# Optimization experiments

Measured on AMD Instinct MI355X. Metric: run time of the kernel, lower is better.

The kernel has to match this reference:

```python
import jax, jax.numpy as jnp
import numpy as np

NEG_INF = -1e10  # matches torch masked_fill_ value -10000000000.0


def setup_inputs() -> dict:
    key = jax.random.key(0)
    kq, kk, kv, kd, km = jax.random.split(key, 5)
    B, H, S, D = 4, 8, 2048, 64
    Q = jax.random.normal(kq, (B, H, S, D), dtype=jnp.float32)
    K = jax.random.normal(kk, (B, H, S, D), dtype=jnp.float32)
    V = jax.random.normal(kv, (B, H, S, D), dtype=jnp.float32)
    dist_factor = jax.random.uniform(kd, (B, H, S, S), dtype=jnp.float32)
    attn_mask = jax.random.randint(km, (B, H, S, S), 0, 2).astype(jnp.bool_)
    return {"Q": Q, "K": K, "V": V, "dist_factor": dist_factor, "attn_mask": attn_mask}


def reference(Q, K, V, dist_factor, attn_mask):
    d_k = K.shape[-1]
    # [B,H,S,S] raw scores, scaled by 1/sqrt(d_k) then by distance factor
    scores = jnp.einsum("bhqd,bhkd->bhqk", Q, K) / np.sqrt(d_k).astype(jnp.float32)
    scores = dist_factor * scores
    scores = jnp.where(attn_mask, jnp.asarray(NEG_INF, scores.dtype), scores)
    attn = jax.nn.softmax(scores, axis=-1)
    context = jnp.einsum("bhqk,bhkd->bhqd", attn, V)
    return (context, attn)
```

## Files before the change

kernel.cpp:

```cpp
#include <hip/hip_runtime.h>


typedef float v4f __attribute__((ext_vector_type(4)));
typedef _Float16 v8h __attribute__((ext_vector_type(8)));

#define SEQ 2048
#define DH  64
#define TQ  8
#define TK  64
#define NKT (SEQ / TK)
#define NBH 32
#define PLANE ((size_t)NBH * NKT * 256)

__device__ inline v8h cvt8(float4 a, float4 b) {
    v8h h;
    h[0] = (_Float16)a.x; h[1] = (_Float16)a.y; h[2] = (_Float16)a.z; h[3] = (_Float16)a.w;
    h[4] = (_Float16)b.x; h[5] = (_Float16)b.y; h[6] = (_Float16)b.z; h[7] = (_Float16)b.w;
    return h;
}

__global__ __launch_bounds__(256)
void prep_kernel(const float* __restrict__ Kg, const float* __restrict__ Vg,
                 v8h* __restrict__ W)
{
    const int kt   = blockIdx.x;
    const int bh   = blockIdx.y;
    const int tid  = (int)threadIdx.x;
    const int wave = tid >> 6;
    const int lane = tid & 63;
    const int quad = lane >> 4;
    const int l16  = lane & 15;
    const int k0   = kt * TK;

    const size_t bh_off = (size_t)bh * SEQ * DH;
    const size_t fi     = ((size_t)bh * NKT + kt) * 256 + tid;

    const float* kr = Kg + bh_off + (size_t)(k0 + wave * 16 + l16) * DH + quad * 8;
    W[fi]         = cvt8(((const float4*)kr)[0], ((const float4*)kr)[1]);
    W[PLANE + fi] = cvt8(((const float4*)(kr + 32))[0], ((const float4*)(kr + 32))[1]);

    const float* vc = Vg + bh_off + (size_t)(k0 + quad * 8) * DH + wave * 16 + l16;
    v8h v0, v1;
#pragma unroll
    for (int j = 0; j < 8; ++j) {
        v0[j] = (_Float16)vc[(size_t)j * DH];
        v1[j] = (_Float16)vc[(size_t)(j + 32) * DH];
    }
    W[2 * PLANE + fi] = v0;
    W[3 * PLANE + fi] = v1;
}

template<bool USE_WS>
__global__ __launch_bounds__(256, 4)
void dsda_kernel(const float* __restrict__ Qg, const float* __restrict__ Kg,
                 const float* __restrict__ Vg, const float* __restrict__ distg,
                 const int* __restrict__ maskg, const v8h* __restrict__ W,
                 float* __restrict__ ctx_out, float* __restrict__ attn_out)
{
    const int qt   = blockIdx.x;
    const int bh   = blockIdx.y;
    const int q0   = qt * TQ;
    const int tid  = (int)threadIdx.x;
    const int wave = tid >> 6;
    const int lane = tid & 63;
    const int quad = lane >> 4;
    const int l16  = lane & 15;

    __shared__ __align__(16) _Float16 e_smem[TQ * SEQ];
    __shared__ float rs[TQ];
    if (tid < TQ) rs[tid] = 0.f;

    const size_t bh_off  = (size_t)bh * SEQ;
    const float* Qb = Qg + bh_off * DH;
    const float* Kb = Kg + bh_off * DH;
    const float* Vb = Vg + bh_off * DH;
    const size_t dm_base = (bh_off + (size_t)q0) * SEQ;

    v8h aq0 = {}, aq1 = {};
    if (l16 < TQ) {
        const float* qrow = Qb + (size_t)(q0 + l16) * DH;
        const float4* p0 = (const float4*)(qrow + quad * 8);
        const float4* p1 = (const float4*)(qrow + 32 + quad * 8);
        aq0 = cvt8(p0[0], p0[1]);
        aq1 = cvt8(p1[0], p1[1]);
    }

    v4f acc_pv = {0.f, 0.f, 0.f, 0.f};
    float rsum[4] = {0.f, 0.f, 0.f, 0.f};
    const size_t fbase = (size_t)bh * NKT * 256 + tid;

#define LOAD_FRAGS(KT, B0, B1, B2, B3) do {                                   \
        const size_t fi_ = fbase + (size_t)(KT) * 256;                        \
        B0 = W[fi_]; B1 = W[PLANE + fi_];                                     \
        B2 = W[2 * PLANE + fi_]; B3 = W[3 * PLANE + fi_];                     \
    } while (0)

#define LOAD_DM(KT, DV, MV) do {                                              \
        if (quad < 2) {                                                       \
            const int kc_ = (KT) * TK + wave * 16 + l16;                      \
            _Pragma("unroll")                                                 \
            for (int r_ = 0; r_ < 4; ++r_) {                                  \
                const size_t idx_ = dm_base + (size_t)(quad * 4 + r_) * SEQ + kc_; \
                DV[r_] = __builtin_nontemporal_load(&distg[idx_]);            \
                MV[r_] = __builtin_nontemporal_load(&maskg[idx_]);            \
            }                                                                 \
        }                                                                     \
    } while (0)

    if constexpr (USE_WS) {
        v8h bk0_c, bk1_c, bv0_c, bv1_c;
        float dv_c[4] = {}; int mv_c[4] = {};
        LOAD_FRAGS(0, bk0_c, bk1_c, bv0_c, bv1_c);
        LOAD_DM(0, dv_c, mv_c);

#pragma unroll 2
        for (int kt = 0; kt < NKT; ++kt) {
            const int k0 = kt * TK;

            const int ktn = (kt + 1 < NKT) ? kt + 1 : 0;
            v8h bk0_n, bk1_n, bv0_n, bv1_n;
            float dv_n[4] = {}; int mv_n[4] = {};
            LOAD_FRAGS(ktn, bk0_n, bk1_n, bv0_n, bv1_n);
            LOAD_DM(ktn, dv_n, mv_n);

            v4f accs = {0.f, 0.f, 0.f, 0.f};
            accs = __builtin_amdgcn_mfma_f32_16x16x32_f16(aq0, bk0_c, accs, 0, 0, 0);
            accs = __builtin_amdgcn_mfma_f32_16x16x32_f16(aq1, bk1_c, accs, 0, 0, 0);

            if (quad < 2) {
                const int kc = k0 + wave * 16 + l16;
#pragma unroll
                for (int r = 0; r < 4; ++r) {
                    const int row = quad * 4 + r;
                    const float sc = accs[r] * 0.125f * dv_c[r];
                    const float e  = mv_c[r] ? 0.f : __expf(sc);
                    rsum[r] += e;
                    *(_Float16*)((char*)e_smem + (row * (SEQ * 2) + ((kc * 2) ^ (row << 4)))) = (_Float16)e;
                }
            }

            asm volatile("s_waitcnt lgkmcnt(0)" ::: "memory");
            __builtin_amdgcn_s_barrier();
            asm volatile("" ::: "memory");

            v8h ap0 = {}, ap1 = {};
            if (l16 < TQ) {
                const int b0 = l16 * (SEQ * 2) + (((k0 + quad * 8) * 2) ^ (l16 << 4));
                const int b1 = l16 * (SEQ * 2) + (((k0 + 32 + quad * 8) * 2) ^ (l16 << 4));
                ap0 = *(const v8h*)((const char*)e_smem + b0);
                ap1 = *(const v8h*)((const char*)e_smem + b1);
            }
            acc_pv = __builtin_amdgcn_mfma_f32_16x16x32_f16(ap0, bv0_c, acc_pv, 0, 0, 0);
            acc_pv = __builtin_amdgcn_mfma_f32_16x16x32_f16(ap1, bv1_c, acc_pv, 0, 0, 0);

            bk0_c = bk0_n; bk1_c = bk1_n; bv0_c = bv0_n; bv1_c = bv1_n;
#pragma unroll
            for (int r = 0; r < 4; ++r) { dv_c[r] = dv_n[r]; mv_c[r] = mv_n[r]; }
        }
    } else {
        for (int kt = 0; kt < NKT; ++kt) {
            const int k0 = kt * TK;
            v8h bk0, bk1, bv0, bv1;
            const float* kr = Kb + (size_t)(k0 + wave * 16 + l16) * DH + quad * 8;
            bk0 = cvt8(((const float4*)kr)[0], ((const float4*)kr)[1]);
            bk1 = cvt8(((const float4*)(kr + 32))[0], ((const float4*)(kr + 32))[1]);
            const float* vc = Vb + (size_t)(k0 + quad * 8) * DH + wave * 16 + l16;
#pragma unroll
            for (int j = 0; j < 8; ++j) {
                bv0[j] = (_Float16)vc[(size_t)j * DH];
                bv1[j] = (_Float16)vc[(size_t)(j + 32) * DH];
            }
            float dv[4] = {}; int mv[4] = {};
            LOAD_DM(kt, dv, mv);

            v4f accs = {0.f, 0.f, 0.f, 0.f};
            accs = __builtin_amdgcn_mfma_f32_16x16x32_f16(aq0, bk0, accs, 0, 0, 0);
            accs = __builtin_amdgcn_mfma_f32_16x16x32_f16(aq1, bk1, accs, 0, 0, 0);

            if (quad < 2) {
                const int kc = k0 + wave * 16 + l16;
#pragma unroll
                for (int r = 0; r < 4; ++r) {
                    const int row = quad * 4 + r;
                    const float sc = accs[r] * 0.125f * dv[r];
                    const float e  = mv[r] ? 0.f : __expf(sc);
                    rsum[r] += e;
                    *(_Float16*)((char*)e_smem + (row * (SEQ * 2) + ((kc * 2) ^ (row << 4)))) = (_Float16)e;
                }
            }
            __syncthreads();

            v8h ap0 = {}, ap1 = {};
            if (l16 < TQ) {
                const int b0 = l16 * (SEQ * 2) + (((k0 + quad * 8) * 2) ^ (l16 << 4));
                const int b1 = l16 * (SEQ * 2) + (((k0 + 32 + quad * 8) * 2) ^ (l16 << 4));
                ap0 = *(const v8h*)((const char*)e_smem + b0);
                ap1 = *(const v8h*)((const char*)e_smem + b1);
            }
            acc_pv = __builtin_amdgcn_mfma_f32_16x16x32_f16(ap0, bv0, acc_pv, 0, 0, 0);
            acc_pv = __builtin_amdgcn_mfma_f32_16x16x32_f16(ap1, bv1, acc_pv, 0, 0, 0);
        }
    }

    if (quad < 2) {
#pragma unroll
        for (int r = 0; r < 4; ++r) {
            float v = rsum[r];
            v += __shfl_xor(v, 1);
            v += __shfl_xor(v, 2);
            v += __shfl_xor(v, 4);
            v += __shfl_xor(v, 8);
            if (l16 == 0) atomicAdd(&rs[quad * 4 + r], v);
        }
    }
    __syncthreads();

    if (quad < 2) {
#pragma unroll
        for (int r = 0; r < 4; ++r) {
            const int row = quad * 4 + r;
            const float inv = 1.f / rs[row];
            ctx_out[(bh_off + (size_t)(q0 + row)) * DH + wave * 16 + l16] = acc_pv[r] * inv;
        }
    }

    {
        const int r  = tid >> 5;
        const int tt = tid & 31;
        const float invr = 1.f / rs[r];
        float* arow = attn_out + dm_base + (size_t)r * SEQ;
#pragma unroll
        for (int c = 0; c < 8; ++c) {
            const int col = c * 256 + tt * 8;
            const int b   = r * (SEQ * 2) + ((col * 2) ^ (r << 4));
            v8h e8 = *(const v8h*)((const char*)e_smem + b);
            v4f f0, f1;
            f0[0] = (float)e8[0] * invr; f0[1] = (float)e8[1] * invr;
            f0[2] = (float)e8[2] * invr; f0[3] = (float)e8[3] * invr;
            f1[0] = (float)e8[4] * invr; f1[1] = (float)e8[5] * invr;
            f1[2] = (float)e8[6] * invr; f1[3] = (float)e8[7] * invr;
            __builtin_nontemporal_store(f0, (v4f*)(arow + col));
            __builtin_nontemporal_store(f1, (v4f*)(arow + col) + 1);
        }
    }
}

extern "C" void kernel_launch(void* const* d_in, const int* in_sizes, int n_in,
                              void* d_out, int out_size, void* d_ws, size_t ws_size,
                              hipStream_t stream) {
    const float* Q    = (const float*)d_in[0];
    const float* K    = (const float*)d_in[1];
    const float* V    = (const float*)d_in[2];
    const float* dist = (const float*)d_in[3];
    const int*   mask = (const int*)d_in[4];

    float* ctx  = (float*)d_out;
    float* attn = (float*)d_out + (size_t)4 * 8 * 2048 * 64;

    const size_t need = 4 * PLANE * sizeof(v8h);
    if (d_ws != nullptr && ws_size >= need) {
        hipLaunchKernelGGL(prep_kernel, dim3(NKT, NBH), dim3(256), 0, stream,
                           K, V, (v8h*)d_ws);
        hipLaunchKernelGGL((dsda_kernel<true>), dim3(SEQ / TQ, NBH), dim3(256), 0, stream,
                           Q, K, V, dist, mask, (const v8h*)d_ws, ctx, attn);
    } else {
        hipLaunchKernelGGL((dsda_kernel<false>), dim3(SEQ / TQ, NBH), dim3(256), 0, stream,
                           Q, K, V, dist, mask, (const v8h*)nullptr, ctx, attn);
    }
}
```

Baseline: 1.401 ms.

## Use 16-row query tiles to fill all MFMA rows

Raises the query tile from 8 to 16 rows so the 16x16 MFMA tiles are fully used rather than half-masked. Each K/V fragment load and prep-buffer read now serves twice as many queries, and the grid is halved. Shared memory per block doubles to 64KB, and launch bounds drop to 2 blocks per CU. That reduces occupancy, which may hurt the latency hiding needed for the streaming dist/mask reads.

```diff
diff --git a/kernel.cpp b/kernel.cpp
--- a/kernel.cpp
+++ b/kernel.cpp
@@ -6,7 +6,7 @@
 
 #define SEQ 2048
 #define DH  64
-#define TQ  8
+#define TQ  16
 #define TK  64
 #define NKT (SEQ / TK)
 #define NBH 32
@@ -51,7 +51,7 @@
 }
 
 template<bool USE_WS>
-__global__ __launch_bounds__(256, 4)
+__global__ __launch_bounds__(256, 2)
 void dsda_kernel(const float* __restrict__ Qg, const float* __restrict__ Kg,
                  const float* __restrict__ Vg, const float* __restrict__ distg,
                  const int* __restrict__ maskg, const v8h* __restrict__ W,
@@ -76,8 +76,8 @@
     const float* Vb = Vg + bh_off * DH;
     const size_t dm_base = (bh_off + (size_t)q0) * SEQ;
 
-    v8h aq0 = {}, aq1 = {};
-    if (l16 < TQ) {
+    v8h aq0, aq1;
+    {
         const float* qrow = Qb + (size_t)(q0 + l16) * DH;
         const float4* p0 = (const float4*)(qrow + quad * 8);
         const float4* p1 = (const float4*)(qrow + 32 + quad * 8);
@@ -96,20 +96,18 @@
     } while (0)
 
 #define LOAD_DM(KT, DV, MV) do {                                              \
-        if (quad < 2) {                                                       \
-            const int kc_ = (KT) * TK + wave * 16 + l16;                      \
-            _Pragma("unroll")                                                 \
-            for (int r_ = 0; r_ < 4; ++r_) {                                  \
-                const size_t idx_ = dm_base + (size_t)(quad * 4 + r_) * SEQ + kc_; \
-                DV[r_] = __builtin_nontemporal_load(&distg[idx_]);            \
-                MV[r_] = __builtin_nontemporal_load(&maskg[idx_]);            \
-            }                                                                 \
+        const int kc_ = (KT) * TK + wave * 16 + l16;                          \
+        _Pragma("unroll")                                                     \
+        for (int r_ = 0; r_ < 4; ++r_) {                                      \
+            const size_t idx_ = dm_base + (size_t)(quad * 4 + r_) * SEQ + kc_; \
+            DV[r_] = __builtin_nontemporal_load(&distg[idx_]);                \
+            MV[r_] = __builtin_nontemporal_load(&maskg[idx_]);                \
         }                                                                     \
     } while (0)
 
     if constexpr (USE_WS) {
         v8h bk0_c, bk1_c, bv0_c, bv1_c;
-        float dv_c[4] = {}; int mv_c[4] = {};
+        float dv_c[4]; int mv_c[4];
         LOAD_FRAGS(0, bk0_c, bk1_c, bv0_c, bv1_c);
         LOAD_DM(0, dv_c, mv_c);
 
@@ -119,7 +117,7 @@
 
             const int ktn = (kt + 1 < NKT) ? kt + 1 : 0;
             v8h bk0_n, bk1_n, bv0_n, bv1_n;
-            float dv_n[4] = {}; int mv_n[4] = {};
+            float dv_n[4]; int mv_n[4];
             LOAD_FRAGS(ktn, bk0_n, bk1_n, bv0_n, bv1_n);
             LOAD_DM(ktn, dv_n, mv_n);
 
@@ -127,7 +125,7 @@
             accs = __builtin_amdgcn_mfma_f32_16x16x32_f16(aq0, bk0_c, accs, 0, 0, 0);
             accs = __builtin_amdgcn_mfma_f32_16x16x32_f16(aq1, bk1_c, accs, 0, 0, 0);
 
-            if (quad < 2) {
+            {
                 const int kc = k0 + wave * 16 + l16;
 #pragma unroll
                 for (int r = 0; r < 4; ++r) {
@@ -135,7 +133,7 @@
                     const float sc = accs[r] * 0.125f * dv_c[r];
                     const float e  = mv_c[r] ? 0.f : __expf(sc);
                     rsum[r] += e;
-                    *(_Float16*)((char*)e_smem + (row * (SEQ * 2) + ((kc * 2) ^ (row << 4)))) = (_Float16)e;
+                    *(_Float16*)((char*)e_smem + (row * (SEQ * 2) + ((kc * 2) ^ ((row & 7) << 4)))) = (_Float16)e;
                 }
             }
 
@@ -143,10 +141,10 @@
             __builtin_amdgcn_s_barrier();
             asm volatile("" ::: "memory");
 
-            v8h ap0 = {}, ap1 = {};
-            if (l16 < TQ) {
-                const int b0 = l16 * (SEQ * 2) + (((k0 + quad * 8) * 2) ^ (l16 << 4));
-                const int b1 = l16 * (SEQ * 2) + (((k0 + 32 + quad * 8) * 2) ^ (l16 << 4));
+            v8h ap0, ap1;
+            {
+                const int b0 = l16 * (SEQ * 2) + (((k0 + quad * 8) * 2) ^ ((l16 & 7) << 4));
+                const int b1 = l16 * (SEQ * 2) + (((k0 + 32 + quad * 8) * 2) ^ ((l16 & 7) << 4));
                 ap0 = *(const v8h*)((const char*)e_smem + b0);
                 ap1 = *(const v8h*)((const char*)e_smem + b1);
             }
@@ -170,14 +168,14 @@
                 bv0[j] = (_Float16)vc[(size_t)j * DH];
                 bv1[j] = (_Float16)vc[(size_t)(j + 32) * DH];
             }
-            float dv[4] = {}; int mv[4] = {};
+            float dv[4]; int mv[4];
             LOAD_DM(kt, dv, mv);
 
             v4f accs = {0.f, 0.f, 0.f, 0.f};
             accs = __builtin_amdgcn_mfma_f32_16x16x32_f16(aq0, bk0, accs, 0, 0, 0);
             accs = __builtin_amdgcn_mfma_f32_16x16x32_f16(aq1, bk1, accs, 0, 0, 0);
 
-            if (quad < 2) {
+            {
                 const int kc = k0 + wave * 16 + l16;
 #pragma unroll
                 for (int r = 0; r < 4; ++r) {
@@ -185,15 +183,15 @@
                     const float sc = accs[r] * 0.125f * dv[r];
                     const float e  = mv[r] ? 0.f : __expf(sc);
                     rsum[r] += e;
-                    *(_Float16*)((char*)e_smem + (row * (SEQ * 2) + ((kc * 2) ^ (row << 4)))) = (_Float16)e;
+                    *(_Float16*)((char*)e_smem + (row * (SEQ * 2) + ((kc * 2) ^ ((row & 7) << 4)))) = (_Float16)e;
                 }
             }
             __syncthreads();
 
-            v8h ap0 = {}, ap1 = {};
-            if (l16 < TQ) {
-                const int b0 = l16 * (SEQ * 2) + (((k0 + quad * 8) * 2) ^ (l16 << 4));
-                const int b1 = l16 * (SEQ * 2) + (((k0 + 32 + quad * 8) * 2) ^ (l16 << 4));
+            v8h ap0, ap1;
+            {
+                const int b0 = l16 * (SEQ * 2) + (((k0 + quad * 8) * 2) ^ ((l16 & 7) << 4));
+                const int b1 = l16 * (SEQ * 2) + (((k0 + 32 + quad * 8) * 2) ^ ((l16 & 7) << 4));
                 ap0 = *(const v8h*)((const char*)e_smem + b0);
                 ap1 = *(const v8h*)((const char*)e_smem + b1);
             }
@@ -202,37 +200,33 @@
         }
     }
 
-    if (quad < 2) {
-#pragma unroll
-        for (int r = 0; r < 4; ++r) {
-            float v = rsum[r];
-            v += __shfl_xor(v, 1);
-            v += __shfl_xor(v, 2);
-            v += __shfl_xor(v, 4);
-            v += __shfl_xor(v, 8);
-            if (l16 == 0) atomicAdd(&rs[quad * 4 + r], v);
-        }
+#pragma unroll
+    for (int r = 0; r < 4; ++r) {
+        float v = rsum[r];
+        v += __shfl_xor(v, 1);
+        v += __shfl_xor(v, 2);
+        v += __shfl_xor(v, 4);
+        v += __shfl_xor(v, 8);
+        if (l16 == 0) atomicAdd(&rs[quad * 4 + r], v);
     }
     __syncthreads();
 
-    if (quad < 2) {
-#pragma unroll
-        for (int r = 0; r < 4; ++r) {
-            const int row = quad * 4 + r;
-            const float inv = 1.f / rs[row];
-            ctx_out[(bh_off + (size_t)(q0 + row)) * DH + wave * 16 + l16] = acc_pv[r] * inv;
-        }
+#pragma unroll
+    for (int r = 0; r < 4; ++r) {
+        const int row = quad * 4 + r;
+        const float inv = 1.f / rs[row];
+        ctx_out[(bh_off + (size_t)(q0 + row)) * DH + wave * 16 + l16] = acc_pv[r] * inv;
     }
 
     {
-        const int r  = tid >> 5;
-        const int tt = tid & 31;
+        const int r  = tid >> 4;
+        const int tt = tid & 15;
         const float invr = 1.f / rs[r];
         float* arow = attn_out + dm_base + (size_t)r * SEQ;
 #pragma unroll
-        for (int c = 0; c < 8; ++c) {
-            const int col = c * 256 + tt * 8;
-            const int b   = r * (SEQ * 2) + ((col * 2) ^ (r << 4));
+        for (int c = 0; c < 16; ++c) {
+            const int col = c * 128 + tt * 8;
+            const int b   = r * (SEQ * 2) + ((col * 2) ^ ((r & 7) << 4));
             v8h e8 = *(const v8h*)((const char*)e_smem + b);
             v4f f0, f1;
             f0[0] = (float)e8[0] * invr; f0[1] = (float)e8[1] * invr;
```

Result: faster. 1.318 ms (-5.9%).
